# Optimization experiments

Measured on AMD Instinct MI355X. Metric: run time of the kernel, lower is better.

## Reference

```python
import jax, jax.numpy as jnp
import numpy as np

EPS = 1e-5

def _bn(x, g, b, m, v):
    # x: [B, C, S]; per-channel affine batchnorm in eval mode
    scale = (g * jax.lax.rsqrt(v + EPS))[None, :, None]
    return (x - m[None, :, None]) * scale + b[None, :, None]

def setup_inputs() -> dict:
    key = jax.random.key(0)
    ks = jax.random.split(key, 32)
    B, C, H, W = 8, 512, 64, 32
    IC = 64        # inter_channel = 512 // 8
    S = H * W      # in_spatial = 2048
    IS = S // 8    # inter_spatial = 256
    DS = IS // 8   # down = 32
    randn = lambda k, shp: jax.random.normal(k, shp, dtype=jnp.float32)
    rand = lambda k, shp: jax.random.uniform(k, shp, dtype=jnp.float32)
    return {
        'x': randn(ks[0], (B, C, H, W)),
        'Wt': randn(ks[1], (IC, C)) * 0.05,
        'tg': rand(ks[2], (IC,)), 'tb': randn(ks[3], (IC,)) * 0.1,
        'tm': randn(ks[4], (IC,)) * 0.1, 'tv': rand(ks[5], (IC,)),
        'Wp': randn(ks[6], (IC, C)) * 0.05,
        'pg': rand(ks[7], (IC,)), 'pb': randn(ks[8], (IC,)) * 0.1,
        'pm': randn(ks[9], (IC,)) * 0.1, 'pv': rand(ks[10], (IC,)),
        'Wgg': randn(ks[11], (IS, 2 * S)) * 0.02,
        'ggg': rand(ks[12], (IS,)), 'ggb': randn(ks[13], (IS,)) * 0.1,
        'ggm': randn(ks[14], (IS,)) * 0.1, 'ggv': rand(ks[15], (IS,)),
        'W1': randn(ks[16], (DS, IS)) * 0.05,
        'w1g': rand(ks[17], (DS,)), 'w1b': randn(ks[18], (DS,)) * 0.1,
        'w1m': randn(ks[19], (DS,)) * 0.1, 'w1v': rand(ks[20], (DS,)),
        'W2': randn(ks[21], (1, DS)) * 0.1,
        'w2g': rand(ks[22], (1,)), 'w2b': randn(ks[23], (1,)) * 0.1,
        'w2m': randn(ks[24], (1,)) * 0.1, 'w2v': rand(ks[25], (1,)),
    }

def reference(x, Wt, tg, tb, tm, tv, Wp, pg, pb, pm, pv,
              Wgg, ggg, ggb, ggm, ggv, W1, w1g, w1b, w1m, w1v,
              W2, w2g, w2b, w2m, w2v):
    B, C, H, W = x.shape
    S = H * W
    xf = x.reshape(B, C, S)
    # theta / phi: 1x1 conv + BN + ReLU -> [B, IC, S]
    theta = jax.nn.relu(_bn(jnp.einsum('oc,bcs->bos', Wt, xf), tg, tb, tm, tv))
    phi = jax.nn.relu(_bn(jnp.einsum('oc,bcs->bos', Wp, xf), pg, pb, pm, pv))
    # spatial affinity: Gs[b,s,t] = sum_c theta[b,c,s] * phi[b,c,t]
    Gs = jnp.einsum('bcs,bct->bst', theta, phi)          # [B, S, S]
    # Gs_in = Gs^T (channels=phi-spatial), Gs_out = Gs (channels=theta-spatial)
    joint = jnp.concatenate([jnp.swapaxes(Gs, 1, 2), Gs], axis=1)  # [B, 2S, S]
    g = jax.nn.relu(_bn(jnp.einsum('oc,bcs->bos', Wgg, joint), ggg, ggb, ggm, ggv))
    y = jax.nn.relu(_bn(jnp.einsum('oc,bcs->bos', W1, g), w1g, w1b, w1m, w1v))
    ys = _bn(jnp.einsum('oc,bcs->bos', W2, y), w2g, w2b, w2m, w2v)  # [B, 1, S]
    gate = jax.nn.sigmoid(ys).reshape(B, 1, H, W)
    return x * gate
```

## Files before the change

kernel.cpp:

```cpp
#include <hip/hip_runtime.h>
#include <math.h>

#define EPS 1e-5f
#define B_ 8
#define C_ 512
#define S_ 2048
#define IC_ 64
#define IS_ 256
#define DS_ 32

#define SZ_T      (S_*C_/2)
#define OFF_THT_H 1024
#define OFF_THT_L (OFF_THT_H + SZ_T)
#define OFF_PHT_H (OFF_THT_L + SZ_T)
#define OFF_PHT_L (OFF_PHT_H + SZ_T)
#define SZ_A      (2*IS_*C_/2)
#define OFF_A_H   (OFF_PHT_L + SZ_T)
#define OFF_A_L   (OFF_A_H + SZ_A)
#define OFF_G     (OFF_A_L + SZ_A)
#define OFF_AP    OFF_G

using short8 = __attribute__((ext_vector_type(8))) short;
using sh4    = __attribute__((ext_vector_type(4))) short;
using f32x4  = __attribute__((ext_vector_type(4))) float;

__device__ __forceinline__ short f2bf(float f) {
  union { float f; unsigned u; } v; v.f = f;
  unsigned r = v.u + 0x7fffu + ((v.u >> 16) & 1u);
  return (short)(r >> 16);
}
__device__ __forceinline__ float bf2f(short h) {
  union { unsigned u; float f; } v;
  v.u = ((unsigned)(unsigned short)h) << 16;
  return v.f;
}
__device__ __forceinline__ void split8arr(const float* f, short8& hi, short8& lo) {
#pragma unroll
  for (int e = 0; e < 8; ++e) {
    short h = f2bf(f[e]);
    hi[e] = h;
    lo[e] = f2bf(f[e] - bf2f(h));
  }
}
__device__ __forceinline__ void split44(float4 a, float4 b, short8& hi, short8& lo) {
  float f[8] = {a.x, a.y, a.z, a.w, b.x, b.y, b.z, b.w};
  split8arr(f, hi, lo);
}

__global__ __launch_bounds__(512) void k1_mfma(
    const float* __restrict__ x, const float* __restrict__ Wt,
    const float* __restrict__ Wp,
    const float* __restrict__ tg, const float* __restrict__ tb,
    const float* __restrict__ tm, const float* __restrict__ tv,
    const float* __restrict__ pg, const float* __restrict__ pb,
    const float* __restrict__ pm, const float* __restrict__ pv,
    float* __restrict__ ws) {
  __shared__ short xh[64 * 72], xlo[64 * 72];
  __shared__ short wh[2][64 * 72], wlo[2][64 * 72];
  __shared__ float cst_l[256];
  const int tid  = threadIdx.x;
  const int lane = tid & 63;
  const int wv   = tid >> 6;
  const int mat  = wv >> 2, sh = wv & 3;
  const int s0   = blockIdx.x * 64;
  const int b    = blockIdx.y;
  const float* xb = x + (size_t)b * C_ * S_;
  const int xs = tid & 63;
  const int xo = tid >> 6;

  if (tid < 64) {
    float a = tg[tid] * rsqrtf(tv[tid] + EPS);
    cst_l[tid] = a; cst_l[64 + tid] = tb[tid] - tm[tid] * a;
    float ap = pg[tid] * rsqrtf(pv[tid] + EPS);
    cst_l[128 + tid] = ap; cst_l[192 + tid] = pb[tid] - pm[tid] * ap;
  }

  float  xr[8];
  float4 wr[2][2];
  f32x4  acc[4];
#pragma unroll
  for (int i = 0; i < 4; ++i) acc[i] = (f32x4){0.f, 0.f, 0.f, 0.f};

#define K1_PF(KC) do {                                                        \
    _Pragma("unroll")                                                         \
    for (int e = 0; e < 8; ++e)                                               \
      xr[e] = xb[(size_t)((KC) + xo * 8 + e) * S_ + s0 + xs];                 \
    _Pragma("unroll")                                                         \
    for (int p = 0; p < 2; ++p) {                                             \
      int q = tid + p * 512;                                                  \
      int mq = q >> 9, m = (q >> 3) & 63, oct = q & 7;                        \
      const float* Wm = mq ? Wp : Wt;                                         \
      wr[p][0] = *(const float4*)&Wm[(size_t)m * C_ + (KC) + oct * 8];        \
      wr[p][1] = *(const float4*)&Wm[(size_t)m * C_ + (KC) + oct * 8 + 4];    \
    } } while (0)

  K1_PF(0);
  for (int c = 0; c < 8; ++c) {
    if (c) __syncthreads();
    {
      short8 hi, lo; split8arr(xr, hi, lo);
      *(short8*)&xh[xs * 72 + xo * 8]  = hi;
      *(short8*)&xlo[xs * 72 + xo * 8] = lo;
    }
#pragma unroll
    for (int p = 0; p < 2; ++p) {
      int q = tid + p * 512;
      int mq = q >> 9, m = (q >> 3) & 63, oct = q & 7;
      short8 hi, lo; split44(wr[p][0], wr[p][1], hi, lo);
      *(short8*)&wh[mq][m * 72 + oct * 8]  = hi;
      *(short8*)&wlo[mq][m * 72 + oct * 8] = lo;
    }
    __syncthreads();
    if (c < 7) K1_PF((c + 1) * 64);
#pragma unroll
    for (int ks = 0; ks < 2; ++ks) {
      const int ko = ks * 32 + ((lane >> 4) << 3);
      short8 bh, bl, ah[4], al[4];
      {
        int r = (sh * 16 + (lane & 15)) * 72 + ko;
        bh = *(const short8*)&xh[r];
        bl = *(const short8*)&xlo[r];
      }
#pragma unroll
      for (int mi = 0; mi < 4; ++mi) {
        int r = (mi * 16 + (lane & 15)) * 72 + ko;
        ah[mi] = *(const short8*)&wh[mat][r];
        al[mi] = *(const short8*)&wlo[mat][r];
      }
#pragma unroll
      for (int mi = 0; mi < 4; ++mi) {
        acc[mi] = __builtin_amdgcn_mfma_f32_16x16x32_bf16(ah[mi], bh, acc[mi], 0, 0, 0);
        acc[mi] = __builtin_amdgcn_mfma_f32_16x16x32_bf16(ah[mi], bl, acc[mi], 0, 0, 0);
        acc[mi] = __builtin_amdgcn_mfma_f32_16x16x32_bf16(al[mi], bh, acc[mi], 0, 0, 0);
      }
    }
  }
#undef K1_PF
  const float* ac = &cst_l[mat * 128];
  short* outH = (short*)(ws + (mat ? OFF_PHT_H : OFF_THT_H));
  short* outL = (short*)(ws + (mat ? OFF_PHT_L : OFF_THT_L));
  const int s = s0 + sh * 16 + (lane & 15);
#pragma unroll
  for (int mi = 0; mi < 4; ++mi) {
    const int m = mi * 16 + ((lane >> 4) << 2);
    float4 sc4 = *(const float4*)&ac[m];
    float4 bi4 = *(const float4*)&ac[64 + m];
    float vals[4];
    vals[0] = fmaxf(sc4.x * acc[mi][0] + bi4.x, 0.f);
    vals[1] = fmaxf(sc4.y * acc[mi][1] + bi4.y, 0.f);
    vals[2] = fmaxf(sc4.z * acc[mi][2] + bi4.z, 0.f);
    vals[3] = fmaxf(sc4.w * acc[mi][3] + bi4.w, 0.f);
    sh4 qh, ql;
#pragma unroll
    for (int e = 0; e < 4; ++e) {
      short h = f2bf(vals[e]);
      qh[e] = h; ql[e] = f2bf(vals[e] - bf2f(h));
    }
    size_t ix = (size_t)s * C_ + b * IC_ + m;
    *(sh4*)&outH[ix] = qh;
    *(sh4*)&outL[ix] = ql;
  }
}

__global__ __launch_bounds__(256) void k2_mfma(
    const float* __restrict__ Wgg, const float* __restrict__ ws,
    float* __restrict__ Ap) {
  __shared__ short nh[64 * 72], nlo[64 * 72];
  __shared__ short oh[128 * 72], olo[128 * 72];
  const int tid  = threadIdx.x;
  const int lane = tid & 63;
  const int wv   = tid >> 6;
  const int n0    = blockIdx.x * 64;
  const int o_blk = blockIdx.y * 128;
  const int mat   = blockIdx.z >> 3;
  const int part  = blockIdx.z & 7;
  const int t0 = part * 256;
  const short* BmH = (const short*)(ws + (mat ? OFF_THT_H : OFF_PHT_H));
  const short* BmL = (const short*)(ws + (mat ? OFF_THT_L : OFF_PHT_L));
  const int xs = tid & 63;
  const int xo = tid >> 6;

  short8 arh[2], arl[2];
  float4 br[4][2];
  f32x4  acc[4][2];
#pragma unroll
  for (int i = 0; i < 4; ++i)
#pragma unroll
    for (int j = 0; j < 2; ++j) acc[i][j] = (f32x4){0.f, 0.f, 0.f, 0.f};

#define K2_PF(KC) do {                                                        \
    _Pragma("unroll")                                                         \
    for (int h = 0; h < 2; ++h) {                                             \
      int oct = xo + h * 4;                                                   \
      _Pragma("unroll")                                                       \
      for (int e = 0; e < 8; ++e) {                                           \
        size_t ix = (size_t)(t0 + (KC) + oct * 8 + e) * C_ + n0 + xs;         \
        arh[h][e] = BmH[ix];                                                  \
        arl[h][e] = BmL[ix];                                                  \
      }                                                                       \
    }                                                                         \
    _Pragma("unroll")                                                         \
    for (int p = 0; p < 4; ++p) {                                             \
      int q = tid + p * 256;                                                  \
      int o = q >> 3, oct = q & 7;                                            \
      const float* src = &Wgg[(size_t)(o_blk + o) * (2 * S_) + mat * S_ +     \
                              t0 + (KC) + oct * 8];                           \
      br[p][0] = *(const float4*)src;                                         \
      br[p][1] = *(const float4*)(src + 4);                                   \
    } } while (0)

  K2_PF(0);
  for (int c = 0; c < 4; ++c) {
    if (c) __syncthreads();
#pragma unroll
    for (int h = 0; h < 2; ++h) {
      int oct = xo + h * 4;
      *(short8*)&nh[xs * 72 + oct * 8]  = arh[h];
      *(short8*)&nlo[xs * 72 + oct * 8] = arl[h];
    }
#pragma unroll
    for (int p = 0; p < 4; ++p) {
      int q = tid + p * 256;
      int o = q >> 3, oct = q & 7;
      short8 hi, lo; split44(br[p][0], br[p][1], hi, lo);
      *(short8*)&oh[o * 72 + oct * 8]  = hi;
      *(short8*)&olo[o * 72 + oct * 8] = lo;
    }
    __syncthreads();
    if (c < 3) K2_PF((c + 1) * 64);
#pragma unroll
    for (int ks = 0; ks < 2; ++ks) {
      const int ko = ks * 32 + ((lane >> 4) << 3);
      short8 ah[4], al[4], bh[2], bl[2];
#pragma unroll
      for (int ni = 0; ni < 4; ++ni) {
        int r = (ni * 16 + (lane & 15)) * 72 + ko;
        ah[ni] = *(const short8*)&nh[r];
        al[ni] = *(const short8*)&nlo[r];
      }
#pragma unroll
      for (int oj = 0; oj < 2; ++oj) {
        int r = (wv * 32 + oj * 16 + (lane & 15)) * 72 + ko;
        bh[oj] = *(const short8*)&oh[r];
        bl[oj] = *(const short8*)&olo[r];
      }
#pragma unroll
      for (int ni = 0; ni < 4; ++ni)
#pragma unroll
        for (int oj = 0; oj < 2; ++oj) {
          acc[ni][oj] = __builtin_amdgcn_mfma_f32_16x16x32_bf16(
              ah[ni], bh[oj], acc[ni][oj], 0, 0, 0);
          acc[ni][oj] = __builtin_amdgcn_mfma_f32_16x16x32_bf16(
              ah[ni], bl[oj], acc[ni][oj], 0, 0, 0);
          acc[ni][oj] = __builtin_amdgcn_mfma_f32_16x16x32_bf16(
              al[ni], bh[oj], acc[ni][oj], 0, 0, 0);
        }
    }
  }
#undef K2_PF
#pragma unroll
  for (int ni = 0; ni < 4; ++ni) {
    const int nq = n0 + ni * 16 + ((lane >> 4) << 2);
#pragma unroll
    for (int oj = 0; oj < 2; ++oj) {
      int o = o_blk + wv * 32 + oj * 16 + (lane & 15);
      float4 q;
      q.x = acc[ni][oj][0]; q.y = acc[ni][oj][1];
      q.z = acc[ni][oj][2]; q.w = acc[ni][oj][3];
      *(float4*)&Ap[((size_t)(part * 2 + mat) * IS_ + o) * C_ + nq] = q;
    }
  }
}

__global__ __launch_bounds__(256) void k2b_reduce(float* __restrict__ ws) {
  int f = blockIdx.x * 256 + threadIdx.x;
  const float4* ap = (const float4*)(ws + OFF_AP);
  float4 s = ap[f];
#pragma unroll
  for (int p = 1; p < 8; ++p) {
    float4 t = ap[f + p * 65536];
    s.x += t.x; s.y += t.y; s.z += t.z; s.w += t.w;
  }
  float vals[4] = {s.x, s.y, s.z, s.w};
  sh4 h4, l4;
#pragma unroll
  for (int e = 0; e < 4; ++e) {
    short h = f2bf(vals[e]);
    h4[e] = h; l4[e] = f2bf(vals[e] - bf2f(h));
  }
  ((sh4*)(ws + OFF_A_H))[f] = h4;
  ((sh4*)(ws + OFF_A_L))[f] = l4;
}

__global__ __launch_bounds__(256) void k3_mfma(
    float* __restrict__ ws,
    const float* __restrict__ gg, const float* __restrict__ gb,
    const float* __restrict__ gm, const float* __restrict__ gv) {
  __shared__ short th[64 * 72], tlo[64 * 72];
  __shared__ short ohh[128 * 72], olo[128 * 72];
  __shared__ float cstg[512];
  const int tid  = threadIdx.x;
  const int lane = tid & 63;
  const int wv   = tid >> 6;
  const int s0    = blockIdx.x * 64;
  const int o_blk = blockIdx.y * 128;
  const int b     = blockIdx.z;
  const short* AH = (const short*)(ws + OFF_A_H);
  const short* AL = (const short*)(ws + OFF_A_L);

  {
    float a = gg[tid] * rsqrtf(gv[tid] + EPS);
    cstg[tid] = a; cstg[256 + tid] = gb[tid] - gm[tid] * a;
  }

  short8 arh[2], arl[2];
  short8 brh[4], brl[4];
  f32x4  acc[4][2];
#pragma unroll
  for (int i = 0; i < 4; ++i)
#pragma unroll
    for (int j = 0; j < 2; ++j) acc[i][j] = (f32x4){0.f, 0.f, 0.f, 0.f};

#define K3_PF(MAT) do {                                                       \
    const short* TH = (const short*)(ws + ((MAT) ? OFF_PHT_H : OFF_THT_H));   \
    const short* TL = (const short*)(ws + ((MAT) ? OFF_PHT_L : OFF_THT_L));   \
    _Pragma("unroll")                                                         \
    for (int p = 0; p < 2; ++p) {                                             \
      int q = tid + p * 256;                                                  \
      int sl = q >> 3, oct = q & 7;                                           \
      size_t ix = (size_t)(s0 + sl) * C_ + b * IC_ + oct * 8;                 \
      arh[p] = *(const short8*)&TH[ix];                                       \
      arl[p] = *(const short8*)&TL[ix];                                       \
    }                                                                         \
    _Pragma("unroll")                                                         \
    for (int p = 0; p < 4; ++p) {                                             \
      int q = tid + p * 256;                                                  \
      int o = q >> 3, oct = q & 7;                                            \
      size_t ix = ((size_t)(MAT) * IS_ + o_blk + o) * C_ + b * IC_ + oct * 8; \
      brh[p] = *(const short8*)&AH[ix];                                       \
      brl[p] = *(const short8*)&AL[ix];                                       \
    } } while (0)

  K3_PF(0);
  for (int c = 0; c < 2; ++c) {
    if (c) __syncthreads();
#pragma unroll
    for (int p = 0; p < 2; ++p) {
      int q = tid + p * 256;
      int sl = q >> 3, oct = q & 7;
      *(short8*)&th[sl * 72 + oct * 8]  = arh[p];
      *(short8*)&tlo[sl * 72 + oct * 8] = arl[p];
    }
#pragma unroll
    for (int p = 0; p < 4; ++p) {
      int q = tid + p * 256;
      int o = q >> 3, oct = q & 7;
      *(short8*)&ohh[o * 72 + oct * 8] = brh[p];
      *(short8*)&olo[o * 72 + oct * 8] = brl[p];
    }
    __syncthreads();
    if (c < 1) K3_PF(1);
#pragma unroll
    for (int ks = 0; ks < 2; ++ks) {
      const int ko = ks * 32 + ((lane >> 4) << 3);
      short8 ah[4], al[4], bh[2], bl[2];
#pragma unroll
      for (int si = 0; si < 4; ++si) {
        int r = (si * 16 + (lane & 15)) * 72 + ko;
        ah[si] = *(const short8*)&th[r];
        al[si] = *(const short8*)&tlo[r];
      }
#pragma unroll
      for (int oj = 0; oj < 2; ++oj) {
        int r = (wv * 32 + oj * 16 + (lane & 15)) * 72 + ko;
        bh[oj] = *(const short8*)&ohh[r];
        bl[oj] = *(const short8*)&olo[r];
      }
#pragma unroll
      for (int si = 0; si < 4; ++si)
#pragma unroll
        for (int oj = 0; oj < 2; ++oj) {
          acc[si][oj] = __builtin_amdgcn_mfma_f32_16x16x32_bf16(
              ah[si], bh[oj], acc[si][oj], 0, 0, 0);
          acc[si][oj] = __builtin_amdgcn_mfma_f32_16x16x32_bf16(
              ah[si], bl[oj], acc[si][oj], 0, 0, 0);
          acc[si][oj] = __builtin_amdgcn_mfma_f32_16x16x32_bf16(
              al[si], bh[oj], acc[si][oj], 0, 0, 0);
        }
    }
  }
#undef K3_PF
  short* g = (short*)(ws + OFF_G);
#pragma unroll
  for (int oj = 0; oj < 2; ++oj) {
    int o = o_blk + wv * 32 + oj * 16 + (lane & 15);
    float sc = cstg[o], bi = cstg[256 + o];
#pragma unroll
    for (int si = 0; si < 4; ++si) {
      int sq = s0 + si * 16 + ((lane >> 4) << 2);
      sh4 q4;
      q4[0] = f2bf(fmaxf(sc * acc[si][oj][0] + bi, 0.f));
      q4[1] = f2bf(fmaxf(sc * acc[si][oj][1] + bi, 0.f));
      q4[2] = f2bf(fmaxf(sc * acc[si][oj][2] + bi, 0.f));
      q4[3] = f2bf(fmaxf(sc * acc[si][oj][3] + bi, 0.f));
      *(sh4*)&g[((size_t)b * IS_ + o) * S_ + sq] = q4;
    }
  }
}

__global__ __launch_bounds__(512) void k4_fused(
    const float* __restrict__ x, const float* __restrict__ W1,
    const float* __restrict__ W2,
    const float* __restrict__ w1g, const float* __restrict__ w1b,
    const float* __restrict__ w1m, const float* __restrict__ w1v,
    const float* __restrict__ w2g, const float* __restrict__ w2b,
    const float* __restrict__ w2m, const float* __restrict__ w2v,
    const float* __restrict__ ws, float* __restrict__ out) {
  __shared__ float lds_g[128 * 36];
  __shared__ float lds_w[32 * 260];
  __shared__ float lds_y[32 * 33];
  __shared__ float lds_gate[32];
  __shared__ float wc[66];
  const int tid = threadIdx.x;
  const int s0  = blockIdx.x * 32;
  const int b   = blockIdx.y;
  const int s   = tid & 31;
  const int og  = tid >> 5;
  const short* gsrc = (const short*)(ws + OFF_G) + (size_t)b * IS_ * S_;

  if (tid < 32) {
    float a = w1g[tid] * rsqrtf(w1v[tid] + EPS);
    wc[tid] = a; wc[32 + tid] = w1b[tid] - w1m[tid] * a;
  } else if (tid == 32) {
    float a = w2g[0] * rsqrtf(w2v[0] + EPS);
    wc[64] = a; wc[65] = w2b[0] - w2m[0] * a;
  }
#pragma unroll
  for (int j = 0; j < 4; ++j) {
    int f = tid + j * 512;
    int row = f >> 6, c4 = f & 63;
    *(float4*)&lds_w[row * 260 + c4 * 4] =
        *(const float4*)&W1[(size_t)row * IS_ + c4 * 4];
  }
  float acc[2] = {};

  for (int half = 0; half < 2; ++half) {
    __syncthreads();
    {
      int row = tid >> 2, oct = tid & 3;
      short8 v = *(const short8*)&gsrc[(size_t)(half * 128 + row) * S_ +
                                       s0 + oct * 8];
      float4 f0 = make_float4(bf2f(v[0]), bf2f(v[1]), bf2f(v[2]), bf2f(v[3]));
      float4 f1 = make_float4(bf2f(v[4]), bf2f(v[5]), bf2f(v[6]), bf2f(v[7]));
      *(float4*)&lds_g[row * 36 + oct * 8]     = f0;
      *(float4*)&lds_g[row * 36 + oct * 8 + 4] = f1;
    }
    __syncthreads();
#pragma unroll
    for (int c4 = 0; c4 < 32; ++c4) {
      float g0 = lds_g[(c4 * 4 + 0) * 36 + s];
      float g1 = lds_g[(c4 * 4 + 1) * 36 + s];
      float g2 = lds_g[(c4 * 4 + 2) * 36 + s];
      float g3 = lds_g[(c4 * 4 + 3) * 36 + s];
#pragma unroll
      for (int j = 0; j < 2; ++j) {
        const float4 w = *(const float4*)&lds_w[(og * 2 + j) * 260 +
                                                half * 128 + c4 * 4];
        acc[j] += g0 * w.x + g1 * w.y + g2 * w.z + g3 * w.w;
      }
    }
  }
#pragma unroll
  for (int j = 0; j < 2; ++j) {
    int o = og * 2 + j;
    float v = wc[o] * acc[j] + wc[32 + o];
    lds_y[o * 33 + s] = v > 0.f ? v : 0.f;
  }
  __syncthreads();
  if (tid < 32) {
    float sum = 0.f;
#pragma unroll
    for (int c = 0; c < 32; ++c) sum += W2[c] * lds_y[c * 33 + tid];
    float ys = wc[64] * sum + wc[65];
    lds_gate[tid] = 1.f / (1.f + expf(-ys));
  }
  __syncthreads();
  const int l = tid & 63, w = tid >> 6;
  const int q4 = (l & 7) * 4;
  const int cl = w * 8 + (l >> 3);
  const float4 gv = *(const float4*)&lds_gate[q4];
  const float* xb = x + (size_t)b * C_ * S_ + s0;
  float* ob = out + (size_t)b * C_ * S_ + s0;
#pragma unroll
  for (int it = 0; it < 8; ++it) {
    int ch = it * 64 + cl;
    const float4 xv = *(const float4*)&xb[(size_t)ch * S_ + q4];
    float4 ov;
    ov.x = xv.x * gv.x; ov.y = xv.y * gv.y;
    ov.z = xv.z * gv.z; ov.w = xv.w * gv.w;
    *(float4*)&ob[(size_t)ch * S_ + q4] = ov;
  }
}

extern "C" void kernel_launch(void* const* d_in, const int* in_sizes, int n_in,
                              void* d_out, int out_size, void* d_ws, size_t ws_size,
                              hipStream_t stream) {
  const float* x   = (const float*)d_in[0];
  const float* Wt  = (const float*)d_in[1];
  const float* tg  = (const float*)d_in[2];
  const float* tb  = (const float*)d_in[3];
  const float* tm  = (const float*)d_in[4];
  const float* tv  = (const float*)d_in[5];
  const float* Wp  = (const float*)d_in[6];
  const float* pg  = (const float*)d_in[7];
  const float* pb  = (const float*)d_in[8];
  const float* pm  = (const float*)d_in[9];
  const float* pv  = (const float*)d_in[10];
  const float* Wgg = (const float*)d_in[11];
  const float* ggg = (const float*)d_in[12];
  const float* ggb = (const float*)d_in[13];
  const float* ggm = (const float*)d_in[14];
  const float* ggv = (const float*)d_in[15];
  const float* W1  = (const float*)d_in[16];
  const float* w1g = (const float*)d_in[17];
  const float* w1b = (const float*)d_in[18];
  const float* w1m = (const float*)d_in[19];
  const float* w1v = (const float*)d_in[20];
  const float* W2  = (const float*)d_in[21];
  const float* w2g = (const float*)d_in[22];
  const float* w2b = (const float*)d_in[23];
  const float* w2m = (const float*)d_in[24];
  const float* w2v = (const float*)d_in[25];
  float* ws  = (float*)d_ws;
  float* out = (float*)d_out;

  k1_mfma<<<dim3(32, 8), 512, 0, stream>>>(
      x, Wt, Wp, tg, tb, tm, tv, pg, pb, pm, pv, ws);
  k2_mfma<<<dim3(8, 2, 16), 256, 0, stream>>>(Wgg, ws, ws + OFF_AP);
  k2b_reduce<<<256, 256, 0, stream>>>(ws);
  k3_mfma<<<dim3(32, 2, 8), 256, 0, stream>>>(ws, ggg, ggb, ggm, ggv);
  k4_fused<<<dim3(64, 8), 512, 0, stream>>>(
      x, W1, W2, w1g, w1b, w1m, w1v, w2g, w2b, w2m, w2v, ws, out);
}
```

Baseline: 67.37 us.

## Double-buffer LDS tiles in GEMM kernels and prefetch x in gate kernel

The two MFMA GEMM kernels now use ping-pong shared-memory buffers. The next tile is staged into the alternate buffer after the current tile's MFMAs, which leaves one barrier per iteration instead of two. The final gate kernel also issues its x loads at kernel start so they overlap the W1/W2 compute. In exchange, LDS use doubles, which may lower occupancy, and registers rise from holding eight float4 values of x.

New measurement: 73.16 us. 1.09x slower.

```diff
diff --git a/kernel.cpp b/kernel.cpp
--- a/kernel.cpp
+++ b/kernel.cpp
@@ -55,8 +55,8 @@
     const float* __restrict__ pg, const float* __restrict__ pb,
     const float* __restrict__ pm, const float* __restrict__ pv,
     float* __restrict__ ws) {
-  __shared__ short xh[64 * 72], xlo[64 * 72];
-  __shared__ short wh[2][64 * 72], wlo[2][64 * 72];
+  __shared__ short xh[2][64 * 72], xlo[2][64 * 72];
+  __shared__ short wh[2][2][64 * 72], wlo[2][2][64 * 72];
   __shared__ float cst_l[256];
   const int tid  = threadIdx.x;
   const int lane = tid & 63;
@@ -94,23 +94,24 @@
       wr[p][1] = *(const float4*)&Wm[(size_t)m * C_ + (KC) + oct * 8 + 4];    \
     } } while (0)
 
+#define K1_STAGE(BUF) do {                                                    \
+    { short8 hi, lo; split8arr(xr, hi, lo);                                   \
+      *(short8*)&xh[BUF][xs * 72 + xo * 8]  = hi;                             \
+      *(short8*)&xlo[BUF][xs * 72 + xo * 8] = lo; }                           \
+    _Pragma("unroll")                                                         \
+    for (int p = 0; p < 2; ++p) {                                             \
+      int q = tid + p * 512;                                                  \
+      int mq = q >> 9, m = (q >> 3) & 63, oct = q & 7;                        \
+      short8 hi, lo; split44(wr[p][0], wr[p][1], hi, lo);                     \
+      *(short8*)&wh[BUF][mq][m * 72 + oct * 8]  = hi;                         \
+      *(short8*)&wlo[BUF][mq][m * 72 + oct * 8] = lo;                         \
+    } } while (0)
+
   K1_PF(0);
+  K1_STAGE(0);
+  __syncthreads();
   for (int c = 0; c < 8; ++c) {
-    if (c) __syncthreads();
-    {
-      short8 hi, lo; split8arr(xr, hi, lo);
-      *(short8*)&xh[xs * 72 + xo * 8]  = hi;
-      *(short8*)&xlo[xs * 72 + xo * 8] = lo;
-    }
-#pragma unroll
-    for (int p = 0; p < 2; ++p) {
-      int q = tid + p * 512;
-      int mq = q >> 9, m = (q >> 3) & 63, oct = q & 7;
-      short8 hi, lo; split44(wr[p][0], wr[p][1], hi, lo);
-      *(short8*)&wh[mq][m * 72 + oct * 8]  = hi;
-      *(short8*)&wlo[mq][m * 72 + oct * 8] = lo;
-    }
-    __syncthreads();
+    const int cb = c & 1;
     if (c < 7) K1_PF((c + 1) * 64);
 #pragma unroll
     for (int ks = 0; ks < 2; ++ks) {
@@ -118,14 +119,14 @@
       short8 bh, bl, ah[4], al[4];
       {
         int r = (sh * 16 + (lane & 15)) * 72 + ko;
-        bh = *(const short8*)&xh[r];
-        bl = *(const short8*)&xlo[r];
+        bh = *(const short8*)&xh[cb][r];
+        bl = *(const short8*)&xlo[cb][r];
       }
 #pragma unroll
       for (int mi = 0; mi < 4; ++mi) {
         int r = (mi * 16 + (lane & 15)) * 72 + ko;
-        ah[mi] = *(const short8*)&wh[mat][r];
-        al[mi] = *(const short8*)&wlo[mat][r];
+        ah[mi] = *(const short8*)&wh[cb][mat][r];
+        al[mi] = *(const short8*)&wlo[cb][mat][r];
       }
 #pragma unroll
       for (int mi = 0; mi < 4; ++mi) {
@@ -134,8 +135,13 @@
         acc[mi] = __builtin_amdgcn_mfma_f32_16x16x32_bf16(al[mi], bh, acc[mi], 0, 0, 0);
       }
     }
+    if (c < 7) {
+      K1_STAGE(cb ^ 1);
+      __syncthreads();
+    }
   }
 #undef K1_PF
+#undef K1_STAGE
   const float* ac = &cst_l[mat * 128];
   short* outH = (short*)(ws + (mat ? OFF_PHT_H : OFF_THT_H));
   short* outL = (short*)(ws + (mat ? OFF_PHT_L : OFF_THT_L));
@@ -165,8 +171,8 @@
 __global__ __launch_bounds__(256) void k2_mfma(
     const float* __restrict__ Wgg, const float* __restrict__ ws,
     float* __restrict__ Ap) {
-  __shared__ short nh[64 * 72], nlo[64 * 72];
-  __shared__ short oh[128 * 72], olo[128 * 72];
+  __shared__ short nh[2][64 * 72], nlo[2][64 * 72];
+  __shared__ short oh[2][128 * 72], olo[2][128 * 72];
   const int tid  = threadIdx.x;
   const int lane = tid & 63;
   const int wv   = tid >> 6;
@@ -209,24 +215,27 @@
       br[p][1] = *(const float4*)(src + 4);                                   \
     } } while (0)
 
+#define K2_STAGE(BUF) do {                                                    \
+    _Pragma("unroll")                                                         \
+    for (int h = 0; h < 2; ++h) {                                             \
+      int oct = xo + h * 4;                                                   \
+      *(short8*)&nh[BUF][xs * 72 + oct * 8]  = arh[h];                        \
+      *(short8*)&nlo[BUF][xs * 72 + oct * 8] = arl[h];                        \
+    }                                                                         \
+    _Pragma("unroll")                                                         \
+    for (int p = 0; p < 4; ++p) {                                             \
+      int q = tid + p * 256;                                                  \
+      int o = q >> 3, oct = q & 7;                                            \
+      short8 hi, lo; split44(br[p][0], br[p][1], hi, lo);                     \
+      *(short8*)&oh[BUF][o * 72 + oct * 8]  = hi;                             \
+      *(short8*)&olo[BUF][o * 72 + oct * 8] = lo;                             \
+    } } while (0)
+
   K2_PF(0);
+  K2_STAGE(0);
+  __syncthreads();
   for (int c = 0; c < 4; ++c) {
-    if (c) __syncthreads();
-#pragma unroll
-    for (int h = 0; h < 2; ++h) {
-      int oct = xo + h * 4;
-      *(short8*)&nh[xs * 72 + oct * 8]  = arh[h];
-      *(short8*)&nlo[xs * 72 + oct * 8] = arl[h];
-    }
-#pragma unroll
-    for (int p = 0; p < 4; ++p) {
-      int q = tid + p * 256;
-      int o = q >> 3, oct = q & 7;
-      short8 hi, lo; split44(br[p][0], br[p][1], hi, lo);
-      *(short8*)&oh[o * 72 + oct * 8]  = hi;
-      *(short8*)&olo[o * 72 + oct * 8] = lo;
-    }
-    __syncthreads();
+    const int cb = c & 1;
     if (c < 3) K2_PF((c + 1) * 64);
 #pragma unroll
     for (int ks = 0; ks < 2; ++ks) {
@@ -235,14 +244,14 @@
 #pragma unroll
       for (int ni = 0; ni < 4; ++ni) {
         int r = (ni * 16 + (lane & 15)) * 72 + ko;
-        ah[ni] = *(const short8*)&nh[r];
-        al[ni] = *(const short8*)&nlo[r];
+        ah[ni] = *(const short8*)&nh[cb][r];
+        al[ni] = *(const short8*)&nlo[cb][r];
       }
 #pragma unroll
       for (int oj = 0; oj < 2; ++oj) {
         int r = (wv * 32 + oj * 16 + (lane & 15)) * 72 + ko;
-        bh[oj] = *(const short8*)&oh[r];
-        bl[oj] = *(const short8*)&olo[r];
+        bh[oj] = *(const short8*)&oh[cb][r];
+        bl[oj] = *(const short8*)&olo[cb][r];
       }
 #pragma unroll
       for (int ni = 0; ni < 4; ++ni)
@@ -256,8 +265,13 @@
               al[ni], bh[oj], acc[ni][oj], 0, 0, 0);
         }
     }
+    if (c < 3) {
+      K2_STAGE(cb ^ 1);
+      __syncthreads();
+    }
   }
 #undef K2_PF
+#undef K2_STAGE
 #pragma unroll
   for (int ni = 0; ni < 4; ++ni) {
     const int nq = n0 + ni * 16 + ((lane >> 4) << 2);
@@ -442,6 +456,16 @@
     *(float4*)&lds_w[row * 260 + c4 * 4] =
         *(const float4*)&W1[(size_t)row * IS_ + c4 * 4];
   }
+  const int l = tid & 63, w = tid >> 6;
+  const int q4 = (l & 7) * 4;
+  const int cl = w * 8 + (l >> 3);
+  const float* xb = x + (size_t)b * C_ * S_ + s0;
+  float* ob = out + (size_t)b * C_ * S_ + s0;
+  float4 xv[8];
+#pragma unroll
+  for (int it = 0; it < 8; ++it)
+    xv[it] = *(const float4*)&xb[(size_t)(it * 64 + cl) * S_ + q4];
+
   float acc[2] = {};
 
   for (int half = 0; half < 2; ++half) {
@@ -464,9 +488,9 @@
       float g3 = lds_g[(c4 * 4 + 3) * 36 + s];
 #pragma unroll
       for (int j = 0; j < 2; ++j) {
-        const float4 w = *(const float4*)&lds_w[(og * 2 + j) * 260 +
-                                                half * 128 + c4 * 4];
-        acc[j] += g0 * w.x + g1 * w.y + g2 * w.z + g3 * w.w;
+        const float4 wv4 = *(const float4*)&lds_w[(og * 2 + j) * 260 +
+                                                  half * 128 + c4 * 4];
+        acc[j] += g0 * wv4.x + g1 * wv4.y + g2 * wv4.z + g3 * wv4.w;
       }
     }
   }
@@ -485,19 +509,13 @@
     lds_gate[tid] = 1.f / (1.f + expf(-ys));
   }
   __syncthreads();
-  const int l = tid & 63, w = tid >> 6;
-  const int q4 = (l & 7) * 4;
-  const int cl = w * 8 + (l >> 3);
   const float4 gv = *(const float4*)&lds_gate[q4];
-  const float* xb = x + (size_t)b * C_ * S_ + s0;
-  float* ob = out + (size_t)b * C_ * S_ + s0;
 #pragma unroll
   for (int it = 0; it < 8; ++it) {
     int ch = it * 64 + cl;
-    const float4 xv = *(const float4*)&xb[(size_t)ch * S_ + q4];
     float4 ov;
-    ov.x = xv.x * gv.x; ov.y = xv.y * gv.y;
-    ov.z = xv.z * gv.z; ov.w = xv.w * gv.w;
+    ov.x = xv[it].x * gv.x; ov.y = xv[it].y * gv.y;
+    ov.z = xv[it].z * gv.z; ov.w = xv[it].w * gv.w;
     *(float4*)&ob[(size_t)ch * S_ + q4] = ov;
   }
 }
```
